# Performance work log

Hardware: AMD Instinct MI355X
Metric: run time of the kernel (lower is better)

The kernel has to match this reference:

```python
import jax, jax.numpy as jnp
import numpy as np

# Constants mirroring FFTGADBase(feature_extractor='none', Npre=2000, block_size=64, overlap=16)
L = 0.24            # diffusion step size l
K_COEF = 0.03       # K = exp(logk), logk = log(0.03) fixed in RGB mode
EPS = 1e-8
BLOCK_SIZE = 64
OVERLAP = 16
NPRE = 2000
FFT_STEPS = 10
VAR_THRESH = 0.1
UNIF_FRAC = 0.7
B, H, W = 2, 1024, 1024
SH, SW = 128, 128


def _g(x, K):
    # Perona-Malik edge-stopping function (repo's g)
    return 1.0 / (1.0 + (x * x) / (K * K))


def _c(feats, K):
    # diffusion coefficients from channel-mean absolute finite differences
    cv = _g(jnp.mean(jnp.abs(feats[:, :, 1:, :] - feats[:, :, :-1, :]), axis=1, keepdims=True), K)
    ch = _g(jnp.mean(jnp.abs(feats[:, :, :, 1:] - feats[:, :, :, :-1]), axis=1, keepdims=True), K)
    return cv, ch  # cv: [B,1,H-1,W], ch: [B,1,H,W-1]


def _diffuse_step(cv, ch, I, l=L):
    # anisotropic diffusion stencil update (transmissions between neighbors)
    dv = I[:, :, 1:, :] - I[:, :, :-1, :]
    dh = I[:, :, :, 1:] - I[:, :, :, :-1]
    tv = l * cv * dv
    th = l * ch * dh
    I = I - jnp.pad(tv, ((0, 0), (0, 0), (1, 0), (0, 0))) + jnp.pad(tv, ((0, 0), (0, 0), (0, 1), (0, 0)))
    I = I - jnp.pad(th, ((0, 0), (0, 0), (0, 0), (1, 0))) + jnp.pad(th, ((0, 0), (0, 0), (0, 0), (0, 1)))
    return I


def _adjust_step(img, source, mask_inv):
    b, c, h, w = img.shape
    sh, sw = source.shape[2], source.shape[3]
    fy, fx = h // sh, w // sw
    # AdaptiveAvgPool2d((sh,sw)) with exact divisor == uniform 8x8 mean pool
    img_ss = img.reshape(b, c, sh, fy, sw, fx).mean(axis=(3, 5))
    ratio_ss = source / (img_ss + EPS)
    ratio_ss = jnp.where(mask_inv, 1.0, ratio_ss)
    # F.interpolate(mode='nearest') with exact multiple == pixel repeat
    ratio = jnp.repeat(jnp.repeat(ratio_ss, fy, axis=2), fx, axis=3)
    return img * ratio


def _avgpool3(x):
    # F.avg_pool2d(x, 3, stride=1, padding=1), count_include_pad=True -> /9 everywhere
    s = jax.lax.reduce_window(x, 0.0, jax.lax.add, (1, 1, 3, 3), (1, 1, 1, 1),
                              [(0, 0), (0, 0), (1, 1), (1, 1)])
    return s / 9.0


def _uniform_regions(cv, ch):
    cv_var = _avgpool3(cv ** 2) - _avgpool3(cv) ** 2
    ch_var = _avgpool3(ch ** 2) - _avgpool3(ch) ** 2
    hm = min(cv_var.shape[2], ch_var.shape[2])
    wm = min(cv_var.shape[3], ch_var.shape[3])
    return (cv_var[:, :, :hm, :wm] < VAR_THRESH) & (ch_var[:, :, :hm, :wm] < VAR_THRESH)


def _fft_block(block, cv_b, ch_b):
    # Closed-form multi-step uniform-coefficient diffusion in the Fourier domain:
    # eigenvalue of one explicit diffusion step on periodic grid, raised to FFT_STEPS.
    cv_m = cv_b.mean(axis=(1, 2, 3), keepdims=True)  # [B,1,1,1]
    ch_m = ch_b.mean(axis=(1, 2, 3), keepdims=True)
    bh, bw = block.shape[-2], block.shape[-1]
    fy = jnp.arange(bh, dtype=jnp.float32)[:, None]
    fx = jnp.arange(bw // 2 + 1, dtype=jnp.float32)[None, :]
    lam = (1.0 - 2.0 * L * cv_m * (1.0 - jnp.cos(2.0 * jnp.pi * fy / bh))
               - 2.0 * L * ch_m * (1.0 - jnp.cos(2.0 * jnp.pi * fx / bw)))
    Fb = jnp.fft.rfft2(block)
    return jnp.fft.irfft2(Fb * (lam ** FFT_STEPS), s=(bh, bw)).astype(block.dtype)


def _fft_diffuse(depth, cv, ch, ur):
    b, c, h, w = depth.shape
    h_cv, w_cv = cv.shape[2], cv.shape[3]
    h_ch, w_ch = ch.shape[2], ch.shape[3]
    step = BLOCK_SIZE - OVERLAP
    for y in range(0, h, step):
        for x in range(0, w, step):
            ye, xe = min(y + BLOCK_SIZE, h), min(x + BLOCK_SIZE, w)
            cye, cxe = min(ye - 1, h_cv), min(xe, w_cv)
            hye, hxe = min(ye, h_ch), min(xe - 1, w_ch)
            if y >= cye or x >= cxe or y >= hye or x >= hxe:
                continue
            uye, uxe = min(ye, ur.shape[2]), min(xe, ur.shape[3])
            if y >= uye or x >= uxe:
                continue
            old = depth[:, :, y:ye, x:xe]
            new = _fft_block(old, cv[:, :, y:cye, x:cxe], ch[:, :, y:hye, x:hxe])
            unif = ur[:, :, y:uye, x:uxe].astype(jnp.float32).mean(axis=(1, 2, 3))
            apply_fft = (unif > UNIF_FRAC)[:, None, None, None]
            bh, bw = ye - y, xe - x
            by = jnp.ones((bh,), dtype=jnp.float32)
            if y > 0:
                n = min(OVERLAP, bh)
                by = by.at[:n].set(jnp.arange(n, dtype=jnp.float32) / OVERLAP)
            bx = jnp.ones((bw,), dtype=jnp.float32)
            if x > 0:
                n = min(OVERLAP, bw)
                bx = bx.at[:n].set(jnp.arange(n, dtype=jnp.float32) / OVERLAP)
            blend = by[:, None] * bx[None, :]
            merged = old * (1.0 - blend) + new * blend  # at (0,0) blend==1 -> direct write, as in torch
            merged = jnp.where(apply_fft, merged, old)
            depth = depth.at[:, :, y:ye, x:xe].set(merged)
    return depth


def _diffuse(img, guide, source, mask_inv):
    # RGB mode: guide_feats = cat([guide, img], 1); K = exp(logk) = 0.03
    feats = jnp.concatenate([guide, img], axis=1)
    cv, ch = _c(feats, K_COEF)
    ur = _uniform_regions(cv, ch)
    # Npre section runs under torch.no_grad()
    img0 = jax.lax.stop_gradient(img)
    cv0 = jax.lax.stop_gradient(cv)
    ch0 = jax.lax.stop_gradient(ch)
    img0 = _fft_diffuse(img0, cv0, ch0, ur)

    def body(I, _):
        I = _diffuse_step(cv0, ch0, I)
        I = _adjust_step(I, jax.lax.stop_gradient(source), mask_inv)
        return I, None

    y_pred, _ = jax.lax.scan(body, img0, None, length=min(500, NPRE))
    return y_pred, cv, ch


def setup_inputs() -> dict:
    key = jax.random.key(0)
    k1, k2, k3, k4 = jax.random.split(key, 4)
    guide = jax.random.normal(k1, (B, 3, H, W), dtype=jnp.float32)
    # keep depths safely > deps=0.1 so the shift branch is statically off
    source = jax.random.uniform(k2, (B, 1, SH, SW), dtype=jnp.float32) + 0.5
    mask_lr = jax.random.uniform(k3, (B, 1, SH, SW), dtype=jnp.float32)
    y_bicubic = jnp.repeat(jnp.repeat(source, H // SH, axis=2), W // SW, axis=3) \
                + 0.05 * jax.random.normal(k4, (B, 1, H, W), dtype=jnp.float32)
    return {"guide": guide, "source": source, "mask_lr": mask_lr, "y_bicubic": y_bicubic}


def reference(guide, source, mask_lr, y_bicubic):
    mask_inv = mask_lr < 0.5
    y_pred, cv, ch = _diffuse(y_bicubic, guide, source, mask_inv)
    return y_pred, cv, ch
```

## Files before the change

### kernel.cpp

```cpp
#include <hip/hip_runtime.h>

#define HH 1024
#define WW 1024
#define HW 1048576
#define NBLK 22

__device__ __forceinline__ float aload(const float* p)
{
    return __uint_as_float(__hip_atomic_load((const unsigned int*)p,
                           __ATOMIC_RELAXED, __HIP_MEMORY_SCOPE_AGENT));
}
__device__ __forceinline__ void astore(float* p, float v)
{
    __hip_atomic_store((unsigned int*)p, __float_as_uint(v),
                       __ATOMIC_RELAXED, __HIP_MEMORY_SCOPE_AGENT);
}

__global__ __launch_bounds__(256) void coeff_kernel(
    const float* __restrict__ guide, const float* __restrict__ img,
    float* __restrict__ cv, float* __restrict__ ch)
{
    int x = blockIdx.x * 256 + threadIdx.x;
    int y = blockIdx.y;
    int b = blockIdx.z;
    const float* g0 = guide + (size_t)b * 3 * HW;
    const float* im = img + (size_t)b * HW;
    int p = y * WW + x;
    float f0 = g0[p], f1 = g0[HW + p], f2 = g0[2 * HW + p], f3 = im[p];
    const float KK = 0.03f * 0.03f;
    if (y < HH - 1) {
        int q = p + WW;
        float s = fabsf(g0[q] - f0) + fabsf(g0[HW + q] - f1)
                + fabsf(g0[2 * HW + q] - f2) + fabsf(im[q] - f3);
        float t = s * 0.25f;
        cv[(size_t)b * 1023 * 1024 + p] = 1.0f / (1.0f + t * t / KK);
    }
    if (x < WW - 1) {
        int q = p + 1;
        float s = fabsf(g0[q] - f0) + fabsf(g0[HW + q] - f1)
                + fabsf(g0[2 * HW + q] - f2) + fabsf(im[q] - f3);
        float t = s * 0.25f;
        ch[(size_t)b * 1024 * 1023 + y * 1023 + x] = 1.0f / (1.0f + t * t / KK);
    }
}

__device__ __forceinline__ float block_reduce(float v, float* tmp)
{
    #pragma unroll
    for (int off = 32; off > 0; off >>= 1) v += __shfl_down(v, off);
    __syncthreads();
    if ((threadIdx.x & 63) == 0) tmp[threadIdx.x >> 6] = v;
    __syncthreads();
    return tmp[0] + tmp[1] + tmp[2] + tmp[3];
}

__global__ __launch_bounds__(256) void stats_kernel(
    const float* __restrict__ cv, const float* __restrict__ ch,
    float* __restrict__ cvmA, float* __restrict__ chmA, float* __restrict__ unifA)
{
    int iy = blockIdx.x, ix = blockIdx.y, b = blockIdx.z;
    int y0 = iy * 48, x0 = ix * 48;
    int ye = min(y0 + 64, HH), xe = min(x0 + 64, WW);
    int bh = ye - y0, bw = xe - x0;
    const float* cvb = cv + (size_t)b * 1023 * 1024;
    const float* chb = ch + (size_t)b * 1024 * 1023;
    int tid = threadIdx.x;

    int cnt_cv = (bh - 1) * bw;
    float s_cv = 0.f;
    for (int k = tid; k < cnt_cv; k += 256) {
        int r = k / bw, c = k - r * bw;
        s_cv += cvb[(y0 + r) * 1024 + x0 + c];
    }
    int cnt_ch = bh * (bw - 1);
    float s_ch = 0.f;
    for (int k = tid; k < cnt_ch; k += 256) {
        int r = k / (bw - 1), c = k - r * (bw - 1);
        s_ch += chb[(y0 + r) * 1023 + x0 + c];
    }
    int uh = min(ye, 1023) - y0, uw = min(xe, 1023) - x0;
    int cnt_u = uh * uw;
    float s_u = 0.f;
    for (int k = tid; k < cnt_u; k += 256) {
        int r = k / uw, c = k - r * uw;
        int py = y0 + r, px = x0 + c;
        float a1 = 0.f, a2 = 0.f;
        #pragma unroll
        for (int dy = -1; dy <= 1; ++dy)
            #pragma unroll
            for (int dx = -1; dx <= 1; ++dx) {
                int yy = py + dy, xx = px + dx;
                if (yy >= 0 && yy < 1023 && xx >= 0 && xx < 1024) {
                    float v = cvb[yy * 1024 + xx]; a1 += v; a2 += v * v;
                }
            }
        float va = a2 * (1.f / 9.f) - (a1 * (1.f / 9.f)) * (a1 * (1.f / 9.f));
        float b1 = 0.f, b2 = 0.f;
        #pragma unroll
        for (int dy = -1; dy <= 1; ++dy)
            #pragma unroll
            for (int dx = -1; dx <= 1; ++dx) {
                int yy = py + dy, xx = px + dx;
                if (yy >= 0 && yy < 1024 && xx >= 0 && xx < 1023) {
                    float v = chb[yy * 1023 + xx]; b1 += v; b2 += v * v;
                }
            }
        float vb = b2 * (1.f / 9.f) - (b1 * (1.f / 9.f)) * (b1 * (1.f / 9.f));
        s_u += (va < 0.1f && vb < 0.1f) ? 1.f : 0.f;
    }

    __shared__ float tmp[4];
    float t_cv = block_reduce(s_cv, tmp);
    float t_ch = block_reduce(s_ch, tmp);
    float t_u  = block_reduce(s_u, tmp);
    if (tid == 0) {
        int bi = (b * NBLK + iy) * NBLK + ix;
        cvmA[bi]  = t_cv / (float)cnt_cv;
        chmA[bi]  = t_ch / (float)cnt_ch;
        unifA[bi] = t_u / (float)cnt_u;
    }
}

__global__ __launch_bounds__(256) void fftblk_kernel(
    float* __restrict__ depth,
    const float* __restrict__ cvmA, const float* __restrict__ chmA,
    const float* __restrict__ unifA, int d, int iy_lo)
{
    int iy = iy_lo + (int)blockIdx.x;
    int ix = d - 2 * iy;
    int b = blockIdx.y;
    int bi = (b * NBLK + iy) * NBLK + ix;
    if (!(unifA[bi] > 0.7f)) return;

    int y0 = iy * 48, x0 = ix * 48;
    int bh = min(64, HH - y0), bw = min(64, WW - x0);
    int npix = bh * bw;
    int bwm = bw - 1, bhm = bh - 1;
    int lw = (bw == 64) ? 6 : 4;
    float av = 0.24f * cvmA[bi];
    float ah = 0.24f * chmA[bi];

    __shared__ float bufA[4096], bufB[4096], bufO[4096];
    float* cur = bufA;
    float* nxt = bufB;
    int tid = threadIdx.x;
    float* gbase = depth + (size_t)b * HW + y0 * WW + x0;

    for (int idx = tid; idx < npix; idx += 256) {
        int i = idx >> lw, j = idx & bwm;
        float v = gbase[i * WW + j];
        cur[idx] = v; bufO[idx] = v;
    }
    __syncthreads();

    for (int it = 0; it < 10; ++it) {
        for (int idx = tid; idx < npix; idx += 256) {
            int i = idx >> lw, j = idx & bwm;
            float c  = cur[idx];
            float up = cur[(((i - 1) & bhm) << lw) | j];
            float dn = cur[(((i + 1) & bhm) << lw) | j];
            float lf = cur[(i << lw) | ((j - 1) & bwm)];
            float rt = cur[(i << lw) | ((j + 1) & bwm)];
            nxt[idx] = c + av * (up + dn - 2.f * c) + ah * (lf + rt - 2.f * c);
        }
        __syncthreads();
        float* t = cur; cur = nxt; nxt = t;
    }

    const float inv16 = 1.f / 16.f;
    for (int idx = tid; idx < npix; idx += 256) {
        int i = idx >> lw, j = idx & bwm;
        float wy = (y0 > 0 && i < 16) ? (float)i * inv16 : 1.f;
        float wx = (x0 > 0 && j < 16) ? (float)j * inv16 : 1.f;
        float w = wy * wx;
        gbase[i * WW + j] = bufO[idx] * (1.f - w) + cur[idx] * w;
    }
}

__global__ __launch_bounds__(256) void fftblk_group(
    float* __restrict__ depth,
    const float* __restrict__ cvmA, const float* __restrict__ chmA,
    const float* __restrict__ unifA, unsigned int* __restrict__ ftags,
    int base)
{
    int rem = base + (int)blockIdx.x;
    int iy = 0, ix = 0;
    for (int d = 0; d < 64; ++d) {
        int lo = (d > 21) ? ((d - 20) >> 1) : 0;
        int hi = ((d >> 1) < 21) ? (d >> 1) : 21;
        int wd = hi - lo + 1;
        if (rem < wd) { iy = lo + rem; ix = d - 2 * iy; break; }
        rem -= wd;
    }
    int b = blockIdx.y;
    int bi = (b * NBLK + iy) * NBLK + ix;
    int tid = threadIdx.x;

    {
        bool act = false; int di = 0, dj = 0;
        if (tid == 0) { act = (ix > 0);            di = iy;     dj = ix - 1; }
        if (tid == 1) { act = (iy > 0 && ix > 0);  di = iy - 1; dj = ix - 1; }
        if (tid == 2) { act = (iy > 0);            di = iy - 1; dj = ix;     }
        if (tid == 3) { act = (iy > 0 && ix < 21); di = iy - 1; dj = ix + 1; }
        if (tid < 4 && act) {
            const unsigned int* tp = ftags + (((b * NBLK + di) * NBLK + dj) << 4);
            int guard = 0;
            while (__hip_atomic_load(tp, __ATOMIC_RELAXED,
                                     __HIP_MEMORY_SCOPE_AGENT) < 1u) {
                if (++guard > (1 << 20)) break;
                __builtin_amdgcn_s_sleep(2);
            }
        }
    }
    __syncthreads();

    bool active = (unifA[bi] > 0.7f);
    if (active) {
        int y0 = iy * 48, x0 = ix * 48;
        int bh = min(64, HH - y0), bw = min(64, WW - x0);
        const int RH = bh >> 4;
        const int RW = bw >> 4;
        float av = 0.24f * cvmA[bi];
        float ah = 0.24f * chmA[bi];

        __shared__ float rT[2][16][65];
        __shared__ float rB[2][16][65];
        __shared__ float cL[2][16][65];
        __shared__ float cR[2][16][65];

        const int ty = tid >> 4, tx = tid & 15;
        float* gbase = depth + (size_t)b * HW + y0 * WW + x0;

        float cur[4][4], orig[4][4];
        #pragma unroll
        for (int r = 0; r < 4; ++r)
            #pragma unroll
            for (int c = 0; c < 4; ++c)
                if (r < RH && c < RW) {
                    float v = aload(gbase + (RH * ty + r) * WW + RW * tx + c);
                    cur[r][c] = v; orig[r][c] = v;
                }

        for (int it = 0; it < 10; ++it) {
            const int p = it & 1;
            #pragma unroll
            for (int c = 0; c < 4; ++c)
                if (c < RW) {
                    rT[p][ty][RW * tx + c] = cur[0][c];
                    rB[p][ty][RW * tx + c] = (RH == 4) ? cur[3][c] : cur[0][c];
                }
            #pragma unroll
            for (int r = 0; r < 4; ++r)
                if (r < RH) {
                    cL[p][tx][RH * ty + r] = cur[r][0];
                    cR[p][tx][RH * ty + r] = (RW == 4) ? cur[r][3] : cur[r][0];
                }
            __syncthreads();

            float nxt[4][4];
            #pragma unroll
            for (int r = 0; r < 4; ++r)
                #pragma unroll
                for (int c = 0; c < 4; ++c)
                    if (r < RH && c < RW) {
                        float ce = cur[r][c];
                        float up = (r > 0) ? cur[r - 1][c]
                                           : rB[p][(ty - 1) & 15][RW * tx + c];
                        float dn = rT[p][(ty + 1) & 15][RW * tx + c];
                        if (r + 1 < 4) { if (r + 1 < RH) dn = cur[r + 1][c]; }
                        float lf = (c > 0) ? cur[r][c - 1]
                                           : cR[p][(tx - 1) & 15][RH * ty + r];
                        float rt = cL[p][(tx + 1) & 15][RH * ty + r];
                        if (c + 1 < 4) { if (c + 1 < RW) rt = cur[r][c + 1]; }
                        nxt[r][c] = ce + av * (up + dn - 2.f * ce)
                                       + ah * (lf + rt - 2.f * ce);
                    }
            #pragma unroll
            for (int r = 0; r < 4; ++r)
                #pragma unroll
                for (int c = 0; c < 4; ++c)
                    if (r < RH && c < RW) cur[r][c] = nxt[r][c];
        }

        const float inv16 = 1.f / 16.f;
        #pragma unroll
        for (int r = 0; r < 4; ++r)
            #pragma unroll
            for (int c = 0; c < 4; ++c)
                if (r < RH && c < RW) {
                    int i = RH * ty + r, j = RW * tx + c;
                    float wy = (y0 > 0 && i < 16) ? (float)i * inv16 : 1.f;
                    float wx = (x0 > 0 && j < 16) ? (float)j * inv16 : 1.f;
                    float w = wy * wx;
                    astore(gbase + i * WW + j,
                           orig[r][c] * (1.f - w) + cur[r][c] * w);
                }
        asm volatile("s_waitcnt vmcnt(0)" ::: "memory");
    }
    __syncthreads();
    if (tid == 0)
        __hip_atomic_store(ftags + (bi << 4), 1u, __ATOMIC_RELAXED,
                           __HIP_MEMORY_SCOPE_AGENT);
}

__global__ __launch_bounds__(256, 4) void iter_kernel(
    const float* __restrict__ Iin, float* __restrict__ Iout,
    const float* __restrict__ cv, const float* __restrict__ ch,
    const float* __restrict__ source, const float* __restrict__ mask)
{
    const int w = blockIdx.x;
    const int xcd = w & 7, j = w >> 3;
    const int grb = xcd * 32 + (j >> 2);
    const int b  = grb >> 7;
    const int r0 = (grb & 127) * 8;
    const int c0 = (j & 3) * 256;
    const int tid = threadIdx.x;
    __shared__ float sI[10][258];
    const float* Ib  = Iin + (size_t)b * HW;
    const float* cvb = cv + (size_t)b * 1023 * 1024;
    const float* chb = ch + (size_t)b * 1024 * 1023;

    for (int k = tid; k < 10 * 258; k += 256) {
        int r = k / 258, c = k - r * 258;
        int gy = r0 - 1 + r, gx = c0 - 1 + c;
        float v = 0.f;
        if (gy >= 0 && gy < HH && gx >= 0 && gx < WW) v = Ib[gy * WW + gx];
        sI[r][c] = v;
    }

    const int gx = c0 + tid;
    float cvv[9];
    #pragma unroll
    for (int k = 0; k < 9; ++k) {
        int gr = r0 - 1 + k;
        cvv[k] = (gr >= 0 && gr < 1023) ? cvb[gr * 1024 + gx] : 0.f;
    }
    float chl[8], chh[8];
    #pragma unroll
    for (int k = 0; k < 8; ++k) {
        int rr = r0 + k;
        chh[k] = (gx < 1023) ? chb[rr * 1023 + gx] : 0.f;
        chl[k] = (gx > 0)    ? chb[rr * 1023 + gx - 1] : 0.f;
    }
    __syncthreads();

    float o[8];
    #pragma unroll
    for (int r = 0; r < 8; ++r) {
        float c  = sI[r + 1][tid + 1];
        float up = sI[r][tid + 1], dn = sI[r + 2][tid + 1];
        float lf = sI[r + 1][tid], rt = sI[r + 1][tid + 2];
        o[r] = c + 0.24f * ( cvv[r + 1] * (dn - c) - cvv[r] * (c - up)
                           + chh[r] * (rt - c)     - chl[r] * (c - lf) );
    }

    float colsum = 0.f;
    #pragma unroll
    for (int r = 0; r < 8; ++r) colsum += o[r];
    colsum += __shfl_xor(colsum, 1);
    colsum += __shfl_xor(colsum, 2);
    colsum += __shfl_xor(colsum, 4);
    float mean = colsum * (1.0f / 64.0f);

    int sy = r0 >> 3;
    int sx = (c0 >> 3) + (tid >> 3);
    int sidx = b * 128 * 128 + sy * 128 + sx;
    float ratio = (mask[sidx] < 0.5f) ? 1.0f : source[sidx] / (mean + 1e-8f);

    float* Ob = Iout + (size_t)b * HW;
    #pragma unroll
    for (int r = 0; r < 8; ++r)
        Ob[(r0 + r) * WW + c0 + tid] = o[r] * ratio;
}

__global__ __launch_bounds__(256, 1) void iter500_strip(
    float* __restrict__ depth,
    const float* __restrict__ cv, const float* __restrict__ ch,
    const float* __restrict__ source, const float* __restrict__ mask,
    float* __restrict__ rowbuf,
    unsigned int* __restrict__ tags,
    int niter)
{
    const int s   = blockIdx.x;
    const int b   = s >> 7;
    const int rb  = s & 127;
    const int r0  = rb * 8;
    const int tid = threadIdx.x;
    const int w   = tid >> 6;
    const int l   = tid & 63;
    const int gx0 = (w << 8) + (l << 2);
    const int swz = (w << 8) + l;

    __shared__ float sE[2][3][2][8];

    float* gdep = depth + (size_t)b * HW;

    float o[8][4];
    #pragma unroll
    for (int r = 0; r < 8; ++r) {
        float4 v = *(const float4*)(gdep + (size_t)(r0 + r) * WW + gx0);
        o[r][0] = v.x; o[r][1] = v.y; o[r][2] = v.z; o[r][3] = v.w;
    }
    unsigned int* mytag = tags + ((s * 4 + w) << 4);
    {
        float* dT = rowbuf + ((size_t)s * 2 + 0) * 1024 + swz;
        float* dB = rowbuf + ((size_t)s * 2 + 1) * 1024 + swz;
        #pragma unroll
        for (int c = 0; c < 4; ++c) { astore(dT + (c << 6), o[0][c]);
                                      astore(dB + (c << 6), o[7][c]); }
        asm volatile("s_waitcnt vmcnt(0)" ::: "memory");
        if (l == 0)
            __hip_atomic_store(mytag, 1u, __ATOMIC_RELAXED, __HIP_MEMORY_SCOPE_AGENT);
    }

    const float* cvb = cv + (size_t)b * 1023 * 1024;
    const float* chb = ch + (size_t)b * 1024 * 1023;
    float cvv[9][4];
    #pragma unroll
    for (int k = 0; k < 9; ++k) {
        int gr = r0 - 1 + k;
        #pragma unroll
        for (int c = 0; c < 4; ++c)
            cvv[k][c] = (gr >= 0 && gr < 1023) ? cvb[(size_t)gr * 1024 + gx0 + c] : 0.f;
    }
    float chh[8][4], chl0[8];
    #pragma unroll
    for (int k = 0; k < 8; ++k) {
        int rr = r0 + k;
        #pragma unroll
        for (int c = 0; c < 4; ++c)
            chh[k][c] = (gx0 + c < 1023) ? chb[(size_t)rr * 1023 + gx0 + c] : 0.f;
        chl0[k] = (gx0 > 0) ? chb[(size_t)rr * 1023 + gx0 - 1] : 0.f;
    }
    int sidx = b * 128 * 128 + rb * 128 + (gx0 >> 3);
    float sval = source[sidx];
    bool  adj  = (mask[sidx] >= 0.5f);

    const unsigned int* tagT = tags + ((((rb > 0   ? s - 1 : s) * 4) + w) << 4);
    const unsigned int* tagB = tags + ((((rb < 127 ? s + 1 : s) * 4) + w) << 4);

    for (int it = 0; it < niter; ++it) {
        const int p = it & 1;
        const int q = p ^ 1;

        if (l == 63 && w < 3) {
            #pragma unroll
            for (int r = 0; r < 8; ++r) sE[p][w][0][r] = o[r][3];
        }
        if (l == 0 && w > 0) {
            #pragma unroll
            for (int r = 0; r < 8; ++r) sE[p][w - 1][1][r] = o[r][0];
        }
        __syncthreads();

        float lfS[8], rtS[8];
        int wl = (w > 0) ? w - 1 : 0;
        int wr = (w < 3) ? w : 0;
        #pragma unroll
        for (int r = 0; r < 8; ++r) {
            float a  = __shfl(o[r][3], l - 1);
            float bq = __shfl(o[r][0], l + 1);
            lfS[r] = (l == 0)  ? ((w > 0) ? sE[p][wl][0][r] : 0.f) : a;
            rtS[r] = (l == 63) ? ((w < 3) ? sE[p][wr][1][r] : 0.f) : bq;
        }

        float n[8][4];
        float cs = 0.f;
        #pragma unroll
        for (int r = 1; r < 7; ++r) {
            #pragma unroll
            for (int c = 0; c < 4; ++c) {
                float cen = o[r][c];
                float up = o[r - 1][c];
                float dn = o[r + 1][c];
                float lf = (c == 0) ? lfS[r] : o[r][c - 1];
                float rt = (c == 3) ? rtS[r] : o[r][c + 1];
                float cl = (c == 0) ? chl0[r] : chh[r][c - 1];
                float v = cen + 0.24f * ( cvv[r + 1][c] * (dn - cen)
                                        - cvv[r][c]     * (cen - up)
                                        + chh[r][c]     * (rt - cen)
                                        - cl            * (cen - lf) );
                n[r][c] = v; cs += v;
            }
        }

        {
            unsigned int target = (unsigned int)(it + 1);
            bool active = (l == 0) ? (rb > 0) : ((l == 1) ? (rb < 127) : false);
            if (active) {
                const unsigned int* pp = (l == 0) ? tagT : tagB;
                int guard = 0;
                while (__hip_atomic_load(pp, __ATOMIC_RELAXED,
                                         __HIP_MEMORY_SCOPE_AGENT) < target) {
                    if (++guard > (1 << 18)) break;
                    __builtin_amdgcn_s_sleep(1);
                }
            }
        }
        asm volatile("" ::: "memory");

        float ht[4] = {0.f, 0.f, 0.f, 0.f}, hb[4] = {0.f, 0.f, 0.f, 0.f};
        if (rb > 0) {
            const float* srcp = rowbuf + (((size_t)p * 256 + (s - 1)) * 2 + 1) * 1024 + swz;
            #pragma unroll
            for (int c = 0; c < 4; ++c) ht[c] = aload(srcp + (c << 6));
        }
        if (rb < 127) {
            const float* srcp = rowbuf + (((size_t)p * 256 + (s + 1)) * 2 + 0) * 1024 + swz;
            #pragma unroll
            for (int c = 0; c < 4; ++c) hb[c] = aload(srcp + (c << 6));
        }

        #pragma unroll
        for (int c = 0; c < 4; ++c) {
            float cen = o[0][c];
            float up = ht[c], dn = o[1][c];
            float lf = (c == 0) ? lfS[0] : o[0][c - 1];
            float rt = (c == 3) ? rtS[0] : o[0][c + 1];
            float cl = (c == 0) ? chl0[0] : chh[0][c - 1];
            float v = cen + 0.24f * ( cvv[1][c] * (dn - cen) - cvv[0][c] * (cen - up)
                                    + chh[0][c] * (rt - cen) - cl * (cen - lf) );
            n[0][c] = v; cs += v;
        }
        #pragma unroll
        for (int c = 0; c < 4; ++c) {
            float cen = o[7][c];
            float up = o[6][c], dn = hb[c];
            float lf = (c == 0) ? lfS[7] : o[7][c - 1];
            float rt = (c == 3) ? rtS[7] : o[7][c + 1];
            float cl = (c == 0) ? chl0[7] : chh[7][c - 1];
            float v = cen + 0.24f * ( cvv[8][c] * (dn - cen) - cvv[7][c] * (cen - up)
                                    + chh[7][c] * (rt - cen) - cl * (cen - lf) );
            n[7][c] = v; cs += v;
        }

        cs += __shfl_xor(cs, 1);
        float mean  = cs * (1.0f / 64.0f);
        float ratio = adj ? sval / (mean + 1e-8f) : 1.0f;
        #pragma unroll
        for (int r = 0; r < 8; ++r)
            #pragma unroll
            for (int c = 0; c < 4; ++c) o[r][c] = n[r][c] * ratio;

        {
            float* dT = rowbuf + (((size_t)q * 256 + s) * 2 + 0) * 1024 + swz;
            float* dB = rowbuf + (((size_t)q * 256 + s) * 2 + 1) * 1024 + swz;
            #pragma unroll
            for (int c = 0; c < 4; ++c) { astore(dT + (c << 6), o[0][c]);
                                          astore(dB + (c << 6), o[7][c]); }
        }
        asm volatile("s_waitcnt vmcnt(0)" ::: "memory");
        if (l == 0)
            __hip_atomic_store(mytag, (unsigned int)(it + 2),
                               __ATOMIC_RELAXED, __HIP_MEMORY_SCOPE_AGENT);
    }

    #pragma unroll
    for (int r = 0; r < 8; ++r) {
        float4 v;
        v.x = o[r][0]; v.y = o[r][1]; v.z = o[r][2]; v.w = o[r][3];
        *(float4*)(gdep + (size_t)(r0 + r) * WW + gx0) = v;
    }
}

extern "C" void kernel_launch(void* const* d_in, const int* in_sizes, int n_in,
                              void* d_out, int out_size, void* d_ws, size_t ws_size,
                              hipStream_t stream)
{
    (void)in_sizes; (void)n_in; (void)out_size; (void)ws_size;
    const float* guide  = (const float*)d_in[0];
    const float* source = (const float*)d_in[1];
    const float* mask   = (const float*)d_in[2];
    const float* ybic   = (const float*)d_in[3];

    float* out   = (float*)d_out;
    float* ypred = out;
    float* cv    = out + 2097152;
    float* ch    = out + 2097152 + 2095104;

    float* wsf    = (float*)d_ws;
    float* dbuf   = wsf;
    float* rowbuf = wsf;
    unsigned int* itags = (unsigned int*)(wsf + 1048576);
    unsigned int* ftags = itags + 16384;
    float* cvmA   = wsf + 2097152;
    float* chmA   = cvmA + 2 * NBLK * NBLK;
    float* unifA  = chmA + 2 * NBLK * NBLK;

    static int persist_ok = -1;
    static int fft_ok = -1;
    static int fgs[16], nfg = 0;
    if (persist_ok < 0) {
        int dev = 0;
        (void)hipGetDevice(&dev);
        hipDeviceProp_t prop;
        int nCU = 0;
        if (hipGetDeviceProperties(&prop, dev) == hipSuccess)
            nCU = prop.multiProcessorCount;
        int nb = 0;
        hipError_t e = hipOccupancyMaxActiveBlocksPerMultiprocessor(
            &nb, iter500_strip, 256, 0);
        persist_ok = (e == hipSuccess && nCU > 0 && nb * nCU >= 256) ? 1 : 0;

        int nb2 = 0;
        hipError_t e2 = hipOccupancyMaxActiveBlocksPerMultiprocessor(
            &nb2, fftblk_group, 256, 0);
        fft_ok = 0;
        if (e2 == hipSuccess && nCU > 0) {
            int capb = (nb2 * nCU) / 2 - 16;
            if (capb >= 64) {
                nfg = 0;
                int start = 0, cnt = 0;
                bool ok = true;
                for (int d = 0; d < 64; ++d) {
                    int lo = (d > 21) ? ((d - 20) >> 1) : 0;
                    int hi = ((d >> 1) < 21) ? (d >> 1) : 21;
                    int wd = hi - lo + 1;
                    if (cnt + wd > capb) {
                        if (nfg >= 15) { ok = false; break; }
                        fgs[nfg * 2] = start; fgs[nfg * 2 + 1] = cnt;
                        ++nfg; start += cnt; cnt = 0;
                    }
                    cnt += wd;
                }
                if (ok && cnt > 0) { fgs[nfg * 2] = start; fgs[nfg * 2 + 1] = cnt; ++nfg; }
                fft_ok = ok ? 1 : 0;
            }
        }
    }

    coeff_kernel<<<dim3(4, HH, 2), 256, 0, stream>>>(guide, ybic, cv, ch);
    stats_kernel<<<dim3(NBLK, NBLK, 2), 256, 0, stream>>>(cv, ch, cvmA, chmA, unifA);
    hipMemcpyAsync(ypred, ybic, (size_t)2 * HW * sizeof(float),
                   hipMemcpyDeviceToDevice, stream);
    hipMemsetAsync(itags, 0, 2 * 16384 * sizeof(unsigned int), stream);

    if (fft_ok) {
        for (int g = 0; g < nfg; ++g)
            fftblk_group<<<dim3(fgs[g * 2 + 1], 2), 256, 0, stream>>>(
                ypred, cvmA, chmA, unifA, ftags, fgs[g * 2]);
    } else {
        for (int d = 0; d <= 3 * (NBLK - 1); ++d) {
            int lo = (d > NBLK - 1) ? (d - NBLK + 2) / 2 : 0;
            int hi = (d / 2 < NBLK - 1) ? d / 2 : NBLK - 1;
            if (lo > hi) continue;
            fftblk_kernel<<<dim3(hi - lo + 1, 2), 256, 0, stream>>>(
                ypred, cvmA, chmA, unifA, d, lo);
        }
    }

    if (persist_ok) {
        iter500_strip<<<dim3(256), 256, 0, stream>>>(
            ypred, cv, ch, source, mask, rowbuf, itags, 500);
    } else {
        for (int i = 0; i < 500; ++i) {
            const float* src = (i & 1) ? dbuf : ypred;
            float*       dst = (i & 1) ? ypred : dbuf;
            iter_kernel<<<dim3(1024), 256, 0, stream>>>(
                src, dst, cv, ch, source, mask);
        }
    }
}
```

Before: 2.074 ms.

## Pack iteration tag with halo values in 64-bit words to remove flag handshake

The persistent 500-iteration strip kernel exchanged halo rows through a float buffer plus a separate per-wave tag, which needed an s_waitcnt drain and a flag store on the producer side and a spin on the flag followed by a second load on the consumer side. Each halo value is now stored as a 64-bit word holding the iteration number in the high half and the float in the low half. Consumers poll the data words directly until every tag matches, so the vmcnt drain and the extra round trip go away. In exchange the halo buffer doubles in size, each poll reads 8 words per lane, and the buffer needs a larger memset per call.

```diff
diff --git a/kernel.cpp b/kernel.cpp
--- a/kernel.cpp
+++ b/kernel.cpp
@@ -14,6 +14,14 @@
 {
     __hip_atomic_store((unsigned int*)p, __float_as_uint(v),
                        __ATOMIC_RELAXED, __HIP_MEMORY_SCOPE_AGENT);
+}
+__device__ __forceinline__ unsigned long long aload64(const unsigned long long* p)
+{
+    return __hip_atomic_load(p, __ATOMIC_RELAXED, __HIP_MEMORY_SCOPE_AGENT);
+}
+__device__ __forceinline__ void astore64(unsigned long long* p, unsigned long long v)
+{
+    __hip_atomic_store(p, v, __ATOMIC_RELAXED, __HIP_MEMORY_SCOPE_AGENT);
 }
 
 __global__ __launch_bounds__(256) void coeff_kernel(
@@ -377,8 +385,7 @@
     float* __restrict__ depth,
     const float* __restrict__ cv, const float* __restrict__ ch,
     const float* __restrict__ source, const float* __restrict__ mask,
-    float* __restrict__ rowbuf,
-    unsigned int* __restrict__ tags,
+    unsigned long long* __restrict__ rowq,
     int niter)
 {
     const int s   = blockIdx.x;
@@ -401,16 +408,15 @@
         float4 v = *(const float4*)(gdep + (size_t)(r0 + r) * WW + gx0);
         o[r][0] = v.x; o[r][1] = v.y; o[r][2] = v.z; o[r][3] = v.w;
     }
-    unsigned int* mytag = tags + ((s * 4 + w) << 4);
     {
-        float* dT = rowbuf + ((size_t)s * 2 + 0) * 1024 + swz;
-        float* dB = rowbuf + ((size_t)s * 2 + 1) * 1024 + swz;
-        #pragma unroll
-        for (int c = 0; c < 4; ++c) { astore(dT + (c << 6), o[0][c]);
-                                      astore(dB + (c << 6), o[7][c]); }
-        asm volatile("s_waitcnt vmcnt(0)" ::: "memory");
-        if (l == 0)
-            __hip_atomic_store(mytag, 1u, __ATOMIC_RELAXED, __HIP_MEMORY_SCOPE_AGENT);
+        unsigned long long* dT = rowq + (((size_t)s * 2 + 0) << 10) + swz;
+        unsigned long long* dB = rowq + (((size_t)s * 2 + 1) << 10) + swz;
+        const unsigned long long tg = 1ull << 32;
+        #pragma unroll
+        for (int c = 0; c < 4; ++c) {
+            astore64(dT + (c << 6), tg | __float_as_uint(o[0][c]));
+            astore64(dB + (c << 6), tg | __float_as_uint(o[7][c]));
+        }
     }
 
     const float* cvb = cv + (size_t)b * 1023 * 1024;
@@ -435,9 +441,6 @@
     int sidx = b * 128 * 128 + rb * 128 + (gx0 >> 3);
     float sval = source[sidx];
     bool  adj  = (mask[sidx] >= 0.5f);
-
-    const unsigned int* tagT = tags + ((((rb > 0   ? s - 1 : s) * 4) + w) << 4);
-    const unsigned int* tagB = tags + ((((rb < 127 ? s + 1 : s) * 4) + w) << 4);
 
     for (int it = 0; it < niter; ++it) {
         const int p = it & 1;
@@ -484,31 +487,46 @@
             }
         }
 
+        float ht[4] = {0.f, 0.f, 0.f, 0.f}, hb[4] = {0.f, 0.f, 0.f, 0.f};
         {
-            unsigned int target = (unsigned int)(it + 1);
-            bool active = (l == 0) ? (rb > 0) : ((l == 1) ? (rb < 127) : false);
-            if (active) {
-                const unsigned int* pp = (l == 0) ? tagT : tagB;
-                int guard = 0;
-                while (__hip_atomic_load(pp, __ATOMIC_RELAXED,
-                                         __HIP_MEMORY_SCOPE_AGENT) < target) {
-                    if (++guard > (1 << 18)) break;
-                    __builtin_amdgcn_s_sleep(1);
-                }
+            const unsigned int want = (unsigned int)(it + 1);
+            const unsigned long long* qT =
+                rowq + ((((size_t)p * 256 + (s - 1)) * 2 + 1) << 10) + swz;
+            const unsigned long long* qB =
+                rowq + ((((size_t)p * 256 + (s + 1)) * 2 + 0) << 10) + swz;
+            int guard = 0;
+            for (;;) {
+                unsigned long long a[4] = {0ull, 0ull, 0ull, 0ull};
+                unsigned long long d[4] = {0ull, 0ull, 0ull, 0ull};
+                if (rb > 0) {
+                    #pragma unroll
+                    for (int c = 0; c < 4; ++c) a[c] = aload64(qT + (c << 6));
+                }
+                if (rb < 127) {
+                    #pragma unroll
+                    for (int c = 0; c < 4; ++c) d[c] = aload64(qB + (c << 6));
+                }
+                bool ok = true;
+                if (rb > 0) {
+                    #pragma unroll
+                    for (int c = 0; c < 4; ++c)
+                        ok = ok && ((unsigned int)(a[c] >> 32) == want);
+                }
+                if (rb < 127) {
+                    #pragma unroll
+                    for (int c = 0; c < 4; ++c)
+                        ok = ok && ((unsigned int)(d[c] >> 32) == want);
+                }
+                if (ok || ++guard > (1 << 16)) {
+                    #pragma unroll
+                    for (int c = 0; c < 4; ++c) {
+                        ht[c] = __uint_as_float((unsigned int)a[c]);
+                        hb[c] = __uint_as_float((unsigned int)d[c]);
+                    }
+                    break;
+                }
+                __builtin_amdgcn_s_sleep(1);
             }
-        }
-        asm volatile("" ::: "memory");
-
-        float ht[4] = {0.f, 0.f, 0.f, 0.f}, hb[4] = {0.f, 0.f, 0.f, 0.f};
-        if (rb > 0) {
-            const float* srcp = rowbuf + (((size_t)p * 256 + (s - 1)) * 2 + 1) * 1024 + swz;
-            #pragma unroll
-            for (int c = 0; c < 4; ++c) ht[c] = aload(srcp + (c << 6));
-        }
-        if (rb < 127) {
-            const float* srcp = rowbuf + (((size_t)p * 256 + (s + 1)) * 2 + 0) * 1024 + swz;
-            #pragma unroll
-            for (int c = 0; c < 4; ++c) hb[c] = aload(srcp + (c << 6));
         }
 
         #pragma unroll
@@ -543,16 +561,17 @@
             for (int c = 0; c < 4; ++c) o[r][c] = n[r][c] * ratio;
 
         {
-            float* dT = rowbuf + (((size_t)q * 256 + s) * 2 + 0) * 1024 + swz;
-            float* dB = rowbuf + (((size_t)q * 256 + s) * 2 + 1) * 1024 + swz;
-            #pragma unroll
-            for (int c = 0; c < 4; ++c) { astore(dT + (c << 6), o[0][c]);
-                                          astore(dB + (c << 6), o[7][c]); }
-        }
-        asm volatile("s_waitcnt vmcnt(0)" ::: "memory");
-        if (l == 0)
-            __hip_atomic_store(mytag, (unsigned int)(it + 2),
-                               __ATOMIC_RELAXED, __HIP_MEMORY_SCOPE_AGENT);
+            unsigned long long* dT =
+                rowq + ((((size_t)q * 256 + s) * 2 + 0) << 10) + swz;
+            unsigned long long* dB =
+                rowq + ((((size_t)q * 256 + s) * 2 + 1) << 10) + swz;
+            const unsigned long long tg = ((unsigned long long)(unsigned int)(it + 2)) << 32;
+            #pragma unroll
+            for (int c = 0; c < 4; ++c) {
+                astore64(dT + (c << 6), tg | __float_as_uint(o[0][c]));
+                astore64(dB + (c << 6), tg | __float_as_uint(o[7][c]));
+            }
+        }
     }
 
     #pragma unroll
@@ -580,12 +599,11 @@
 
     float* wsf    = (float*)d_ws;
     float* dbuf   = wsf;
-    float* rowbuf = wsf;
-    unsigned int* itags = (unsigned int*)(wsf + 1048576);
-    unsigned int* ftags = itags + 16384;
+    unsigned long long* rowq = (unsigned long long*)d_ws;
     float* cvmA   = wsf + 2097152;
     float* chmA   = cvmA + 2 * NBLK * NBLK;
     float* unifA  = chmA + 2 * NBLK * NBLK;
+    unsigned int* ftags = (unsigned int*)(unifA + 2 * NBLK * NBLK);
 
     static int persist_ok = -1;
     static int fft_ok = -1;
@@ -633,7 +651,9 @@
     stats_kernel<<<dim3(NBLK, NBLK, 2), 256, 0, stream>>>(cv, ch, cvmA, chmA, unifA);
     hipMemcpyAsync(ypred, ybic, (size_t)2 * HW * sizeof(float),
                    hipMemcpyDeviceToDevice, stream);
-    hipMemsetAsync(itags, 0, 2 * 16384 * sizeof(unsigned int), stream);
+    hipMemsetAsync(ftags, 0, 16384 * sizeof(unsigned int), stream);
+    if (persist_ok)
+        hipMemsetAsync(rowq, 0, (size_t)2 * 256 * 2 * 1024 * 8, stream);
 
     if (fft_ok) {
         for (int g = 0; g < nfg; ++g)
@@ -651,7 +671,7 @@
 
     if (persist_ok) {
         iter500_strip<<<dim3(256), 256, 0, stream>>>(
-            ypred, cv, ch, source, mask, rowbuf, itags, 500);
+            ypred, cv, ch, source, mask, rowq, 500);
     } else {
         for (int i = 0; i < 500; ++i) {
             const float* src = (i & 1) ? dbuf : ypred;
```

Result: slower. 2.181 ms (+5.2%).

## Launch all FFT blocks in one grid and prefetch non-overlap pixels before dependency wait

Applied to the files above, without the earlier changes.

Replaces the multi-launch grouped or per-diagonal FFT block scheduling with a single 484x2 launch that relies on the inter-block tag dependencies. Each block now loads the pixels outside the 16-pixel overlap region before spinning on its neighbours, and only loads the overlap pixels after the wait. The s_sleep in the spin loop is removed and the guard limit raised. This cuts launch overhead and hides load latency, but a single grid with spin-waits assumes forward progress across all resident blocks and risks deadlock or a guard timeout if dependent blocks are not co-resident. The occupancy check that made this safe has been removed.

```diff
diff --git a/kernel.cpp b/kernel.cpp
--- a/kernel.cpp
+++ b/kernel.cpp
@@ -121,62 +121,6 @@
     }
 }
 
-__global__ __launch_bounds__(256) void fftblk_kernel(
-    float* __restrict__ depth,
-    const float* __restrict__ cvmA, const float* __restrict__ chmA,
-    const float* __restrict__ unifA, int d, int iy_lo)
-{
-    int iy = iy_lo + (int)blockIdx.x;
-    int ix = d - 2 * iy;
-    int b = blockIdx.y;
-    int bi = (b * NBLK + iy) * NBLK + ix;
-    if (!(unifA[bi] > 0.7f)) return;
-
-    int y0 = iy * 48, x0 = ix * 48;
-    int bh = min(64, HH - y0), bw = min(64, WW - x0);
-    int npix = bh * bw;
-    int bwm = bw - 1, bhm = bh - 1;
-    int lw = (bw == 64) ? 6 : 4;
-    float av = 0.24f * cvmA[bi];
-    float ah = 0.24f * chmA[bi];
-
-    __shared__ float bufA[4096], bufB[4096], bufO[4096];
-    float* cur = bufA;
-    float* nxt = bufB;
-    int tid = threadIdx.x;
-    float* gbase = depth + (size_t)b * HW + y0 * WW + x0;
-
-    for (int idx = tid; idx < npix; idx += 256) {
-        int i = idx >> lw, j = idx & bwm;
-        float v = gbase[i * WW + j];
-        cur[idx] = v; bufO[idx] = v;
-    }
-    __syncthreads();
-
-    for (int it = 0; it < 10; ++it) {
-        for (int idx = tid; idx < npix; idx += 256) {
-            int i = idx >> lw, j = idx & bwm;
-            float c  = cur[idx];
-            float up = cur[(((i - 1) & bhm) << lw) | j];
-            float dn = cur[(((i + 1) & bhm) << lw) | j];
-            float lf = cur[(i << lw) | ((j - 1) & bwm)];
-            float rt = cur[(i << lw) | ((j + 1) & bwm)];
-            nxt[idx] = c + av * (up + dn - 2.f * c) + ah * (lf + rt - 2.f * c);
-        }
-        __syncthreads();
-        float* t = cur; cur = nxt; nxt = t;
-    }
-
-    const float inv16 = 1.f / 16.f;
-    for (int idx = tid; idx < npix; idx += 256) {
-        int i = idx >> lw, j = idx & bwm;
-        float wy = (y0 > 0 && i < 16) ? (float)i * inv16 : 1.f;
-        float wx = (x0 > 0 && j < 16) ? (float)j * inv16 : 1.f;
-        float w = wy * wx;
-        gbase[i * WW + j] = bufO[idx] * (1.f - w) + cur[idx] * w;
-    }
-}
-
 __global__ __launch_bounds__(256) void fftblk_group(
     float* __restrict__ depth,
     const float* __restrict__ cvmA, const float* __restrict__ chmA,
@@ -195,6 +139,29 @@
     int b = blockIdx.y;
     int bi = (b * NBLK + iy) * NBLK + ix;
     int tid = threadIdx.x;
+
+    bool active = (unifA[bi] > 0.7f);
+    int y0 = iy * 48, x0 = ix * 48;
+    int bh = min(64, HH - y0), bw = min(64, WW - x0);
+    const int RH = bh >> 4;
+    const int RW = bw >> 4;
+    const int ty = tid >> 4, tx = tid & 15;
+    float* gbase = depth + (size_t)b * HW + y0 * WW + x0;
+
+    float cur[4][4], orig[4][4];
+    if (active) {
+        #pragma unroll
+        for (int r = 0; r < 4; ++r)
+            #pragma unroll
+            for (int c = 0; c < 4; ++c)
+                if (r < RH && c < RW) {
+                    int i = RH * ty + r, j = RW * tx + c;
+                    if (i >= 16 && j >= 16) {
+                        float v = aload(gbase + i * WW + j);
+                        cur[r][c] = v; orig[r][c] = v;
+                    }
+                }
+    }
 
     {
         bool act = false; int di = 0, dj = 0;
@@ -207,39 +174,32 @@
             int guard = 0;
             while (__hip_atomic_load(tp, __ATOMIC_RELAXED,
                                      __HIP_MEMORY_SCOPE_AGENT) < 1u) {
-                if (++guard > (1 << 20)) break;
-                __builtin_amdgcn_s_sleep(2);
+                if (++guard > (1 << 22)) break;
             }
         }
     }
     __syncthreads();
 
-    bool active = (unifA[bi] > 0.7f);
     if (active) {
-        int y0 = iy * 48, x0 = ix * 48;
-        int bh = min(64, HH - y0), bw = min(64, WW - x0);
-        const int RH = bh >> 4;
-        const int RW = bw >> 4;
         float av = 0.24f * cvmA[bi];
         float ah = 0.24f * chmA[bi];
+
+        #pragma unroll
+        for (int r = 0; r < 4; ++r)
+            #pragma unroll
+            for (int c = 0; c < 4; ++c)
+                if (r < RH && c < RW) {
+                    int i = RH * ty + r, j = RW * tx + c;
+                    if (i < 16 || j < 16) {
+                        float v = aload(gbase + i * WW + j);
+                        cur[r][c] = v; orig[r][c] = v;
+                    }
+                }
 
         __shared__ float rT[2][16][65];
         __shared__ float rB[2][16][65];
         __shared__ float cL[2][16][65];
         __shared__ float cR[2][16][65];
-
-        const int ty = tid >> 4, tx = tid & 15;
-        float* gbase = depth + (size_t)b * HW + y0 * WW + x0;
-
-        float cur[4][4], orig[4][4];
-        #pragma unroll
-        for (int r = 0; r < 4; ++r)
-            #pragma unroll
-            for (int c = 0; c < 4; ++c)
-                if (r < RH && c < RW) {
-                    float v = aload(gbase + (RH * ty + r) * WW + RW * tx + c);
-                    cur[r][c] = v; orig[r][c] = v;
-                }
 
         for (int it = 0; it < 10; ++it) {
             const int p = it & 1;
@@ -588,8 +548,6 @@
     float* unifA  = chmA + 2 * NBLK * NBLK;
 
     static int persist_ok = -1;
-    static int fft_ok = -1;
-    static int fgs[16], nfg = 0;
     if (persist_ok < 0) {
         int dev = 0;
         (void)hipGetDevice(&dev);
@@ -601,32 +559,6 @@
         hipError_t e = hipOccupancyMaxActiveBlocksPerMultiprocessor(
             &nb, iter500_strip, 256, 0);
         persist_ok = (e == hipSuccess && nCU > 0 && nb * nCU >= 256) ? 1 : 0;
-
-        int nb2 = 0;
-        hipError_t e2 = hipOccupancyMaxActiveBlocksPerMultiprocessor(
-            &nb2, fftblk_group, 256, 0);
-        fft_ok = 0;
-        if (e2 == hipSuccess && nCU > 0) {
-            int capb = (nb2 * nCU) / 2 - 16;
-            if (capb >= 64) {
-                nfg = 0;
-                int start = 0, cnt = 0;
-                bool ok = true;
-                for (int d = 0; d < 64; ++d) {
-                    int lo = (d > 21) ? ((d - 20) >> 1) : 0;
-                    int hi = ((d >> 1) < 21) ? (d >> 1) : 21;
-                    int wd = hi - lo + 1;
-                    if (cnt + wd > capb) {
-                        if (nfg >= 15) { ok = false; break; }
-                        fgs[nfg * 2] = start; fgs[nfg * 2 + 1] = cnt;
-                        ++nfg; start += cnt; cnt = 0;
-                    }
-                    cnt += wd;
-                }
-                if (ok && cnt > 0) { fgs[nfg * 2] = start; fgs[nfg * 2 + 1] = cnt; ++nfg; }
-                fft_ok = ok ? 1 : 0;
-            }
-        }
     }
 
     coeff_kernel<<<dim3(4, HH, 2), 256, 0, stream>>>(guide, ybic, cv, ch);
@@ -635,19 +567,8 @@
                    hipMemcpyDeviceToDevice, stream);
     hipMemsetAsync(itags, 0, 2 * 16384 * sizeof(unsigned int), stream);
 
-    if (fft_ok) {
-        for (int g = 0; g < nfg; ++g)
-            fftblk_group<<<dim3(fgs[g * 2 + 1], 2), 256, 0, stream>>>(
-                ypred, cvmA, chmA, unifA, ftags, fgs[g * 2]);
-    } else {
-        for (int d = 0; d <= 3 * (NBLK - 1); ++d) {
-            int lo = (d > NBLK - 1) ? (d - NBLK + 2) / 2 : 0;
-            int hi = (d / 2 < NBLK - 1) ? d / 2 : NBLK - 1;
-            if (lo > hi) continue;
-            fftblk_kernel<<<dim3(hi - lo + 1, 2), 256, 0, stream>>>(
-                ypred, cvmA, chmA, unifA, d, lo);
-        }
-    }
+    fftblk_group<<<dim3(484, 2), 256, 0, stream>>>(
+        ypred, cvmA, chmA, unifA, ftags, 0);
 
     if (persist_ok) {
         iter500_strip<<<dim3(256), 256, 0, stream>>>(
```

Result: slower. 2.146 ms (+3.5%).

## Add per-diagonal wavefront front counter and prefetch non-overlap pixels before waiting

Applied to the files above, without the earlier changes.

Each FFT-block group block now loads its non-overlap pixels before waiting on its dependencies, so that global load latency is hidden behind the wait. Only the overlap-region pixels, which neighbouring blocks write, are loaded after the dependency wait. A per-batch diagonal completion counter and front index are added. Each block first waits until the front reaches the previous diagonal, then does the existing per-neighbour tag wait with a shorter sleep. The new counters add atomic traffic and a serial front-advance loop, and they carry a risk of ordering subtleties because the atomics are relaxed.

```diff
diff --git a/kernel.cpp b/kernel.cpp
--- a/kernel.cpp
+++ b/kernel.cpp
@@ -14,6 +14,12 @@
 {
     __hip_atomic_store((unsigned int*)p, __float_as_uint(v),
                        __ATOMIC_RELAXED, __HIP_MEMORY_SCOPE_AGENT);
+}
+__device__ __forceinline__ int diag_width(int d)
+{
+    int lo = (d > 21) ? ((d - 20) >> 1) : 0;
+    int hi = ((d >> 1) < 21) ? (d >> 1) : 21;
+    return hi - lo + 1;
 }
 
 __global__ __launch_bounds__(256) void coeff_kernel(
@@ -181,21 +187,56 @@
     float* __restrict__ depth,
     const float* __restrict__ cvmA, const float* __restrict__ chmA,
     const float* __restrict__ unifA, unsigned int* __restrict__ ftags,
+    unsigned int* __restrict__ fdcnt, unsigned int* __restrict__ ffront,
     int base)
 {
     int rem = base + (int)blockIdx.x;
     int iy = 0, ix = 0;
     for (int d = 0; d < 64; ++d) {
-        int lo = (d > 21) ? ((d - 20) >> 1) : 0;
-        int hi = ((d >> 1) < 21) ? (d >> 1) : 21;
-        int wd = hi - lo + 1;
-        if (rem < wd) { iy = lo + rem; ix = d - 2 * iy; break; }
+        int wd = diag_width(d);
+        if (rem < wd) {
+            int lo = (d > 21) ? ((d - 20) >> 1) : 0;
+            iy = lo + rem; ix = d - 2 * iy; break;
+        }
         rem -= wd;
     }
     int b = blockIdx.y;
     int bi = (b * NBLK + iy) * NBLK + ix;
     int tid = threadIdx.x;
-
+    const int dD = 2 * iy + ix;
+
+    bool active = (unifA[bi] > 0.7f);
+    int y0 = iy * 48, x0 = ix * 48;
+    int bh = min(64, HH - y0), bw = min(64, WW - x0);
+    const int RH = bh >> 4;
+    const int RW = bw >> 4;
+    const int ty = tid >> 4, tx = tid & 15;
+    float* gbase = depth + (size_t)b * HW + y0 * WW + x0;
+
+    float cur[4][4], orig[4][4];
+    if (active) {
+        #pragma unroll
+        for (int r = 0; r < 4; ++r)
+            #pragma unroll
+            for (int c = 0; c < 4; ++c)
+                if (r < RH && c < RW) {
+                    int i = RH * ty + r, j = RW * tx + c;
+                    if ((i >= 16 || iy == 0) && (j >= 16 || ix == 0)) {
+                        float v = gbase[i * WW + j];
+                        cur[r][c] = v; orig[r][c] = v;
+                    }
+                }
+    }
+
+    if (tid == 0 && dD >= 2) {
+        const unsigned int* fp = ffront + (b << 4);
+        int guard = 0;
+        while ((int)__hip_atomic_load(fp, __ATOMIC_RELAXED,
+                                      __HIP_MEMORY_SCOPE_AGENT) < dD - 1) {
+            if (++guard > (1 << 14)) break;
+            __builtin_amdgcn_s_sleep(64);
+        }
+    }
     {
         bool act = false; int di = 0, dj = 0;
         if (tid == 0) { act = (ix > 0);            di = iy;     dj = ix - 1; }
@@ -208,38 +249,32 @@
             while (__hip_atomic_load(tp, __ATOMIC_RELAXED,
                                      __HIP_MEMORY_SCOPE_AGENT) < 1u) {
                 if (++guard > (1 << 20)) break;
-                __builtin_amdgcn_s_sleep(2);
+                __builtin_amdgcn_s_sleep(1);
             }
         }
     }
     __syncthreads();
 
-    bool active = (unifA[bi] > 0.7f);
     if (active) {
-        int y0 = iy * 48, x0 = ix * 48;
-        int bh = min(64, HH - y0), bw = min(64, WW - x0);
-        const int RH = bh >> 4;
-        const int RW = bw >> 4;
         float av = 0.24f * cvmA[bi];
         float ah = 0.24f * chmA[bi];
+
+        #pragma unroll
+        for (int r = 0; r < 4; ++r)
+            #pragma unroll
+            for (int c = 0; c < 4; ++c)
+                if (r < RH && c < RW) {
+                    int i = RH * ty + r, j = RW * tx + c;
+                    if ((iy > 0 && i < 16) || (ix > 0 && j < 16)) {
+                        float v = aload(gbase + i * WW + j);
+                        cur[r][c] = v; orig[r][c] = v;
+                    }
+                }
 
         __shared__ float rT[2][16][65];
         __shared__ float rB[2][16][65];
         __shared__ float cL[2][16][65];
         __shared__ float cR[2][16][65];
-
-        const int ty = tid >> 4, tx = tid & 15;
-        float* gbase = depth + (size_t)b * HW + y0 * WW + x0;
-
-        float cur[4][4], orig[4][4];
-        #pragma unroll
-        for (int r = 0; r < 4; ++r)
-            #pragma unroll
-            for (int c = 0; c < 4; ++c)
-                if (r < RH && c < RW) {
-                    float v = aload(gbase + (RH * ty + r) * WW + RW * tx + c);
-                    cur[r][c] = v; orig[r][c] = v;
-                }
 
         for (int it = 0; it < 10; ++it) {
             const int p = it & 1;
@@ -298,9 +333,23 @@
         asm volatile("s_waitcnt vmcnt(0)" ::: "memory");
     }
     __syncthreads();
-    if (tid == 0)
+    if (tid == 0) {
         __hip_atomic_store(ftags + (bi << 4), 1u, __ATOMIC_RELAXED,
                            __HIP_MEMORY_SCOPE_AGENT);
+        unsigned int old = __hip_atomic_fetch_add(fdcnt + ((b * 64 + dD) << 4),
+                               1u, __ATOMIC_RELAXED, __HIP_MEMORY_SCOPE_AGENT);
+        if ((int)old + 1 == diag_width(dD)) {
+            for (int dd = dD; dd < 64; ++dd) {
+                if (__hip_atomic_load(ffront + (b << 4), __ATOMIC_RELAXED,
+                        __HIP_MEMORY_SCOPE_AGENT) != (unsigned int)dd) break;
+                if (__hip_atomic_load(fdcnt + ((b * 64 + dd) << 4),
+                        __ATOMIC_RELAXED, __HIP_MEMORY_SCOPE_AGENT)
+                        != (unsigned int)diag_width(dd)) break;
+                __hip_atomic_store(ffront + (b << 4), (unsigned int)(dd + 1),
+                        __ATOMIC_RELAXED, __HIP_MEMORY_SCOPE_AGENT);
+            }
+        }
+    }
 }
 
 __global__ __launch_bounds__(256, 4) void iter_kernel(
@@ -581,8 +630,10 @@
     float* wsf    = (float*)d_ws;
     float* dbuf   = wsf;
     float* rowbuf = wsf;
-    unsigned int* itags = (unsigned int*)(wsf + 1048576);
-    unsigned int* ftags = itags + 16384;
+    unsigned int* itags  = (unsigned int*)(wsf + 1048576);
+    unsigned int* ftags  = itags + 16384;
+    unsigned int* fdcnt  = ftags + 16384;
+    unsigned int* ffront = fdcnt + 2048;
     float* cvmA   = wsf + 2097152;
     float* chmA   = cvmA + 2 * NBLK * NBLK;
     float* unifA  = chmA + 2 * NBLK * NBLK;
@@ -633,12 +684,13 @@
     stats_kernel<<<dim3(NBLK, NBLK, 2), 256, 0, stream>>>(cv, ch, cvmA, chmA, unifA);
     hipMemcpyAsync(ypred, ybic, (size_t)2 * HW * sizeof(float),
                    hipMemcpyDeviceToDevice, stream);
-    hipMemsetAsync(itags, 0, 2 * 16384 * sizeof(unsigned int), stream);
+    hipMemsetAsync(itags, 0, (16384 + 16384 + 2048 + 32) * sizeof(unsigned int),
+                   stream);
 
     if (fft_ok) {
         for (int g = 0; g < nfg; ++g)
             fftblk_group<<<dim3(fgs[g * 2 + 1], 2), 256, 0, stream>>>(
-                ypred, cvmA, chmA, unifA, ftags, fgs[g * 2]);
+                ypred, cvmA, chmA, unifA, ftags, fdcnt, ffront, fgs[g * 2]);
     } else {
         for (int d = 0; d <= 3 * (NBLK - 1); ++d) {
             int lo = (d > NBLK - 1) ? (d - NBLK + 2) / 2 : 0;
```

Result: slower. 2.132 ms (+2.8%).
